# Kernel tuning notes

Measured on AMD Instinct MI355X. Metric: run time of the kernel, lower is better.

The kernel has to match this reference:

```python
import jax, jax.numpy as jnp
import numpy as np

DEGREE = 7

def setup_inputs() -> dict:
    key = jax.random.key(0)
    k1, k2 = jax.random.split(key)
    input_dims, output_dims = 1024, 1024
    x = jax.random.normal(k1, (8192, input_dims), dtype=jnp.float32)
    std = 1.0 / (input_dims * (DEGREE + 1))
    lucas_coeffs = std * jax.random.normal(k2, (input_dims, output_dims, DEGREE + 1), dtype=jnp.float32)
    return {"x": x, "lucas_coeffs": lucas_coeffs}

def reference(x, lucas_coeffs):
    input_dims = lucas_coeffs.shape[0]
    x = x.reshape(-1, input_dims)
    x = jnp.tanh(x)
    # Lucas polynomial recurrence: L0=2, L1=x, L_i = x*L_{i-1} + L_{i-2}
    basis = [jnp.full_like(x, 2.0)]
    if DEGREE > 0:
        basis.append(x)
    for i in range(2, DEGREE + 1):
        basis.append(x * basis[-1] + basis[-2])
    lucas = jnp.stack(basis, axis=-1)  # [b, i, d]
    y = jnp.einsum('bid,iod->bo', lucas, lucas_coeffs)
    return y
```

## Files before the change

### kernel.cpp

```cpp
#include <hip/hip_runtime.h>
#include <hip/hip_bf16.h>


typedef __attribute__((ext_vector_type(8)))  short  short8;
typedef __attribute__((ext_vector_type(4)))  unsigned short ushort4v;
typedef __attribute__((ext_vector_type(8)))  unsigned short ushort8;
typedef __attribute__((ext_vector_type(4)))  float  float4v;
typedef __attribute__((ext_vector_type(4)))  unsigned int uint4v;

#define M_DIM 8192
#define I_DIM 1024
#define O_DIM 1024
#define K_DIM 8192
#define BM 64
#define BN 128
#define BK 64
#define NSTEP (K_DIM / BK)

__device__ __forceinline__ unsigned short f2bf(float f) {
    unsigned int u = __float_as_uint(f);
    u += 0x7FFFu + ((u >> 16) & 1u);
    return (unsigned short)(u >> 16);
}

__global__ __launch_bounds__(256) void prep_t_kernel(const float* __restrict__ x,
                                                     unsigned short* __restrict__ T) {
    int idx = (blockIdx.x * 256 + threadIdx.x) * 4;
    float4v v = *(const float4v*)(x + idx);
    ushort4v o;
    o[0] = f2bf(tanhf(v[0]));
    o[1] = f2bf(tanhf(v[1]));
    o[2] = f2bf(tanhf(v[2]));
    o[3] = f2bf(tanhf(v[3]));
    *(ushort4v*)(T + idx) = o;
}

__global__ __launch_bounds__(256) void prep_b_kernel(const float* __restrict__ c,
                                                     unsigned short* __restrict__ Bt) {
    int idx = blockIdx.x * 256 + threadIdx.x;
    int i = idx >> 10;
    int o = idx & 1023;
    const float* src = c + (size_t)i * 8192 + o * 8;
    float4v lo = *(const float4v*)(src);
    float4v hi = *(const float4v*)(src + 4);
    ushort8 v;
    v[0] = f2bf(lo[0]); v[1] = f2bf(lo[1]); v[2] = f2bf(lo[2]); v[3] = f2bf(lo[3]);
    v[4] = f2bf(hi[0]); v[5] = f2bf(hi[1]); v[6] = f2bf(hi[2]); v[7] = f2bf(hi[3]);
    *(ushort8*)(Bt + (size_t)o * K_DIM + i * 8) = v;
}

__device__ __forceinline__ short8 lucas_frag(unsigned int tb) {
    const float t = __uint_as_float(tb << 16);
    const float L2v = fmaf(t, t, 2.0f);
    const float L3v = fmaf(t, L2v, t);
    const float L4v = fmaf(t, L3v, L2v);
    const float L5v = fmaf(t, L4v, L3v);
    const float L6v = fmaf(t, L5v, L4v);
    const float L7v = fmaf(t, L6v, L5v);
    const unsigned int u2 = __float_as_uint(L2v) + 0x8000u;
    const unsigned int u3 = __float_as_uint(L3v) + 0x8000u;
    const unsigned int u4 = __float_as_uint(L4v) + 0x8000u;
    const unsigned int u5 = __float_as_uint(L5v) + 0x8000u;
    const unsigned int u6 = __float_as_uint(L6v) + 0x8000u;
    const unsigned int u7 = __float_as_uint(L7v) + 0x8000u;
    union { uint4v u; short8 s; } r;
    r.u[0] = 0x4000u | (tb << 16);
    r.u[1] = __builtin_amdgcn_perm(u3, u2, 0x07060302);
    r.u[2] = __builtin_amdgcn_perm(u5, u4, 0x07060302);
    r.u[3] = __builtin_amdgcn_perm(u7, u6, 0x07060302);
    return r.s;
}

__global__ __launch_bounds__(256, 4) void gemm_kernel(const unsigned short* __restrict__ T,
                                                      const unsigned short* __restrict__ Bt,
                                                      float* __restrict__ out) {
    __shared__ unsigned short Bs[2][BN * BK];
    __shared__ unsigned short Ts[2][BM * 8];

    const int tid  = threadIdx.x;
    const int lane = tid & 63;
    const int wave = tid >> 6;
    const int m0 = blockIdx.x * BM;
    const int n0 = blockIdx.y * BN;

    const int wm0  = (wave >> 1) * 32;
    const int wn0  = (wave & 1) * 64;
    const int l16  = lane & 15;
    const int quad = lane >> 4;

    const int srow   = lane >> 3;
    const int il     = lane & 7;
    const int gchunk = il ^ srow;

    float4v acc[2][4];
    const float4v zero = {0.f, 0.f, 0.f, 0.f};
    #pragma unroll
    for (int a = 0; a < 2; ++a)
        #pragma unroll
        for (int b = 0; b < 4; ++b) acc[a][b] = zero;

    #pragma unroll
    for (int r = 0; r < 4; ++r) {
        const int rowb = r * 32 + wave * 8;
        const unsigned short* gB = Bt + (size_t)(n0 + rowb + srow) * K_DIM + gchunk * 8;
        __builtin_amdgcn_global_load_lds(
            (const __attribute__((address_space(1))) unsigned int*)gB,
            (__attribute__((address_space(3))) unsigned int*)&Bs[0][rowb * BK], 16, 0, 0);
    }
    if (wave == 0) {
        const unsigned short* gT = T + (size_t)(m0 + lane) * I_DIM;
        __builtin_amdgcn_global_load_lds(
            (const __attribute__((address_space(1))) unsigned int*)gT,
            (__attribute__((address_space(3))) unsigned int*)&Ts[0][0], 16, 0, 0);
    }
    __syncthreads();

    int cur = 0;
    for (int s = 0; s < NSTEP; ++s) {
        const int nxt = cur ^ 1;

        if (s + 1 < NSTEP) {
            const int kt = (s + 1) * BK;
            #pragma unroll
            for (int r = 0; r < 4; ++r) {
                const int rowb = r * 32 + wave * 8;
                const unsigned short* gB = Bt + (size_t)(n0 + rowb + srow) * K_DIM + kt + gchunk * 8;
                __builtin_amdgcn_global_load_lds(
                    (const __attribute__((address_space(1))) unsigned int*)gB,
                    (__attribute__((address_space(3))) unsigned int*)&Bs[nxt][rowb * BK], 16, 0, 0);
            }
            if (wave == 0) {
                const unsigned short* gT = T + (size_t)(m0 + lane) * I_DIM + kt / 8;
                __builtin_amdgcn_global_load_lds(
                    (const __attribute__((address_space(1))) unsigned int*)gT,
                    (__attribute__((address_space(3))) unsigned int*)&Ts[nxt][0], 16, 0, 0);
            }
        }

        unsigned int tb[2][2];
        #pragma unroll
        for (int tt = 0; tt < 2; ++tt)
            #pragma unroll
            for (int k2 = 0; k2 < 2; ++k2)
                tb[tt][k2] = Ts[cur][(wm0 + tt * 16 + l16) * 8 + (k2 * 4 + quad)];

        #pragma unroll
        for (int k2 = 0; k2 < 2; ++k2) {
            short8 af[2];
            af[0] = lucas_frag(tb[0][k2]);
            af[1] = lucas_frag(tb[1][k2]);
            short8 bfr[4];
            #pragma unroll
            for (int tn = 0; tn < 4; ++tn) {
                const int brow = wn0 + tn * 16 + l16;
                bfr[tn] = *(const short8*)&Bs[cur][brow * BK + (((k2 * 4 + quad) ^ (l16 & 7)) * 8)];
            }
            #pragma unroll
            for (int tt = 0; tt < 2; ++tt)
                #pragma unroll
                for (int tn = 0; tn < 4; ++tn)
                    acc[tt][tn] = __builtin_amdgcn_mfma_f32_16x16x32_bf16(
                        af[tt], bfr[tn], acc[tt][tn], 0, 0, 0);
        }

        __syncthreads();
        cur = nxt;
    }

    #pragma unroll
    for (int tt = 0; tt < 2; ++tt) {
        #pragma unroll
        for (int tn = 0; tn < 4; ++tn) {
            const int col = n0 + wn0 + tn * 16 + l16;
            #pragma unroll
            for (int r = 0; r < 4; ++r) {
                const int row = m0 + wm0 + tt * 16 + quad * 4 + r;
                out[(size_t)row * O_DIM + col] = acc[tt][tn][r];
            }
        }
    }
}

__global__ __launch_bounds__(256) void naive_kernel(const float* __restrict__ x,
                                                    const float* __restrict__ c,
                                                    float* __restrict__ out) {
    int idx = blockIdx.x * 256 + threadIdx.x;
    int b = idx >> 10;
    int o = idx & 1023;
    const float* xb = x + (size_t)b * I_DIM;
    float acc = 0.f;
    for (int i = 0; i < I_DIM; ++i) {
        float t = tanhf(xb[i]);
        float L[8];
        L[0] = 2.0f; L[1] = t;
        #pragma unroll
        for (int d = 2; d < 8; ++d) L[d] = t * L[d - 1] + L[d - 2];
        const float* cc = c + (size_t)i * 8192 + o * 8;
        #pragma unroll
        for (int d = 0; d < 8; ++d) acc += L[d] * cc[d];
    }
    out[idx] = acc;
}

extern "C" void kernel_launch(void* const* d_in, const int* in_sizes, int n_in,
                              void* d_out, int out_size, void* d_ws, size_t ws_size,
                              hipStream_t stream) {
    const float* x      = (const float*)d_in[0];
    const float* coeffs = (const float*)d_in[1];
    float* out = (float*)d_out;

    const size_t btBytes = (size_t)O_DIM * K_DIM * sizeof(unsigned short);
    const size_t tBytes  = (size_t)M_DIM * I_DIM * sizeof(unsigned short);

    if (ws_size >= btBytes + tBytes) {
        unsigned short* Bt = (unsigned short*)d_ws;
        unsigned short* T  = (unsigned short*)((char*)d_ws + btBytes);

        prep_b_kernel<<<(I_DIM * O_DIM) / 256, 256, 0, stream>>>(coeffs, Bt);
        prep_t_kernel<<<(M_DIM * I_DIM) / (4 * 256), 256, 0, stream>>>(x, T);

        dim3 grid(M_DIM / BM, O_DIM / BN);
        gemm_kernel<<<grid, 256, 0, stream>>>(T, Bt, out);
    } else {
        naive_kernel<<<(M_DIM * O_DIM) / 256, 256, 0, stream>>>(x, coeffs, out);
    }
}
```

Baseline: 268.5 us.

## Fuse prep kernels, pack T pairs, use hardware bf16 convert, swap grid order

Merges the two preprocessing kernels into one launch, with the T part writing 8 values per thread interleaved so each lane reads both of its k-chunks with one 32-bit LDS load. Lucas fragment packing uses the hardware packed bf16 conversion when the builtin exists, replacing the add-and-permute truncation. The GEMM grid is transposed so consecutive blocks share the same T rows across N tiles, which changes L2 reuse. The goal is fewer launches, fewer LDS reads and ALU ops in the inner loop, at the cost of a more intricate T layout and a rounding mode that differs slightly from the old one.

```diff
diff --git a/kernel.cpp b/kernel.cpp
--- a/kernel.cpp
+++ b/kernel.cpp
@@ -23,30 +23,37 @@
     return (unsigned short)(u >> 16);
 }
 
-__global__ __launch_bounds__(256) void prep_t_kernel(const float* __restrict__ x,
-                                                     unsigned short* __restrict__ T) {
-    int idx = (blockIdx.x * 256 + threadIdx.x) * 4;
-    float4v v = *(const float4v*)(x + idx);
-    ushort4v o;
-    o[0] = f2bf(tanhf(v[0]));
-    o[1] = f2bf(tanhf(v[1]));
-    o[2] = f2bf(tanhf(v[2]));
-    o[3] = f2bf(tanhf(v[3]));
-    *(ushort4v*)(T + idx) = o;
-}
-
-__global__ __launch_bounds__(256) void prep_b_kernel(const float* __restrict__ c,
-                                                     unsigned short* __restrict__ Bt) {
-    int idx = blockIdx.x * 256 + threadIdx.x;
-    int i = idx >> 10;
-    int o = idx & 1023;
-    const float* src = c + (size_t)i * 8192 + o * 8;
-    float4v lo = *(const float4v*)(src);
-    float4v hi = *(const float4v*)(src + 4);
-    ushort8 v;
-    v[0] = f2bf(lo[0]); v[1] = f2bf(lo[1]); v[2] = f2bf(lo[2]); v[3] = f2bf(lo[3]);
-    v[4] = f2bf(hi[0]); v[5] = f2bf(hi[1]); v[6] = f2bf(hi[2]); v[7] = f2bf(hi[3]);
-    *(ushort8*)(Bt + (size_t)o * K_DIM + i * 8) = v;
+__global__ __launch_bounds__(256) void prep_kernel(const float* __restrict__ x,
+                                                   const float* __restrict__ c,
+                                                   unsigned short* __restrict__ T,
+                                                   unsigned short* __restrict__ Bt) {
+    int bid = blockIdx.x;
+    const int tPart = (M_DIM * I_DIM) / (8 * 256);
+    if (bid < tPart) {
+        int idx = (bid * 256 + threadIdx.x) * 8;
+        float4v v0 = *(const float4v*)(x + idx);
+        float4v v1 = *(const float4v*)(x + idx + 4);
+        unsigned short t[8];
+        t[0] = f2bf(tanhf(v0[0])); t[1] = f2bf(tanhf(v0[1]));
+        t[2] = f2bf(tanhf(v0[2])); t[3] = f2bf(tanhf(v0[3]));
+        t[4] = f2bf(tanhf(v1[0])); t[5] = f2bf(tanhf(v1[1]));
+        t[6] = f2bf(tanhf(v1[2])); t[7] = f2bf(tanhf(v1[3]));
+        ushort8 o;
+        #pragma unroll
+        for (int p = 0; p < 4; ++p) { o[2 * p] = t[p]; o[2 * p + 1] = t[p + 4]; }
+        *(ushort8*)(T + idx) = o;
+    } else {
+        int idx = (bid - tPart) * 256 + threadIdx.x;
+        int i = idx >> 10;
+        int o = idx & 1023;
+        const float* src = c + (size_t)i * 8192 + o * 8;
+        float4v lo = *(const float4v*)(src);
+        float4v hi = *(const float4v*)(src + 4);
+        ushort8 v;
+        v[0] = f2bf(lo[0]); v[1] = f2bf(lo[1]); v[2] = f2bf(lo[2]); v[3] = f2bf(lo[3]);
+        v[4] = f2bf(hi[0]); v[5] = f2bf(hi[1]); v[6] = f2bf(hi[2]); v[7] = f2bf(hi[3]);
+        *(ushort8*)(Bt + (size_t)o * K_DIM + i * 8) = v;
+    }
 }
 
 __device__ __forceinline__ short8 lucas_frag(unsigned int tb) {
@@ -57,17 +64,26 @@
     const float L5v = fmaf(t, L4v, L3v);
     const float L6v = fmaf(t, L5v, L4v);
     const float L7v = fmaf(t, L6v, L5v);
-    const unsigned int u2 = __float_as_uint(L2v) + 0x8000u;
-    const unsigned int u3 = __float_as_uint(L3v) + 0x8000u;
-    const unsigned int u4 = __float_as_uint(L4v) + 0x8000u;
-    const unsigned int u5 = __float_as_uint(L5v) + 0x8000u;
-    const unsigned int u6 = __float_as_uint(L6v) + 0x8000u;
-    const unsigned int u7 = __float_as_uint(L7v) + 0x8000u;
     union { uint4v u; short8 s; } r;
-    r.u[0] = 0x4000u | (tb << 16);
-    r.u[1] = __builtin_amdgcn_perm(u3, u2, 0x07060302);
-    r.u[2] = __builtin_amdgcn_perm(u5, u4, 0x07060302);
-    r.u[3] = __builtin_amdgcn_perm(u7, u6, 0x07060302);
+#if __has_builtin(__builtin_amdgcn_cvt_pk_bf16_f32)
+    {
+        auto p0 = __builtin_amdgcn_cvt_pk_bf16_f32(2.0f, t);
+        auto p1 = __builtin_amdgcn_cvt_pk_bf16_f32(L2v, L3v);
+        auto p2 = __builtin_amdgcn_cvt_pk_bf16_f32(L4v, L5v);
+        auto p3 = __builtin_amdgcn_cvt_pk_bf16_f32(L6v, L7v);
+        __builtin_memcpy(&r.u[0], &p0, 4);
+        __builtin_memcpy(&r.u[1], &p1, 4);
+        __builtin_memcpy(&r.u[2], &p2, 4);
+        __builtin_memcpy(&r.u[3], &p3, 4);
+    }
+#else
+    {
+        r.u[0] = 0x4000u | (tb << 16);
+        r.u[1] = __builtin_amdgcn_perm(__float_as_uint(L3v), __float_as_uint(L2v), 0x07060302);
+        r.u[2] = __builtin_amdgcn_perm(__float_as_uint(L5v), __float_as_uint(L4v), 0x07060302);
+        r.u[3] = __builtin_amdgcn_perm(__float_as_uint(L7v), __float_as_uint(L6v), 0x07060302);
+    }
+#endif
     return r.s;
 }
 
@@ -80,8 +96,8 @@
     const int tid  = threadIdx.x;
     const int lane = tid & 63;
     const int wave = tid >> 6;
-    const int m0 = blockIdx.x * BM;
-    const int n0 = blockIdx.y * BN;
+    const int n0 = blockIdx.x * BN;
+    const int m0 = blockIdx.y * BM;
 
     const int wm0  = (wave >> 1) * 32;
     const int wn0  = (wave & 1) * 64;
@@ -137,18 +153,16 @@
             }
         }
 
-        unsigned int tb[2][2];
+        unsigned int tw[2];
         #pragma unroll
         for (int tt = 0; tt < 2; ++tt)
-            #pragma unroll
-            for (int k2 = 0; k2 < 2; ++k2)
-                tb[tt][k2] = Ts[cur][(wm0 + tt * 16 + l16) * 8 + (k2 * 4 + quad)];
+            tw[tt] = *(const unsigned int*)&Ts[cur][(wm0 + tt * 16 + l16) * 8 + quad * 2];
 
         #pragma unroll
         for (int k2 = 0; k2 < 2; ++k2) {
             short8 af[2];
-            af[0] = lucas_frag(tb[0][k2]);
-            af[1] = lucas_frag(tb[1][k2]);
+            af[0] = lucas_frag(k2 ? (tw[0] >> 16) : (tw[0] & 0xffffu));
+            af[1] = lucas_frag(k2 ? (tw[1] >> 16) : (tw[1] & 0xffffu));
             short8 bfr[4];
             #pragma unroll
             for (int tn = 0; tn < 4; ++tn) {
@@ -216,10 +230,11 @@
         unsigned short* Bt = (unsigned short*)d_ws;
         unsigned short* T  = (unsigned short*)((char*)d_ws + btBytes);
 
-        prep_b_kernel<<<(I_DIM * O_DIM) / 256, 256, 0, stream>>>(coeffs, Bt);
-        prep_t_kernel<<<(M_DIM * I_DIM) / (4 * 256), 256, 0, stream>>>(x, T);
-
-        dim3 grid(M_DIM / BM, O_DIM / BN);
+        const int tBlocks = (M_DIM * I_DIM) / (8 * 256);
+        const int bBlocks = (I_DIM * O_DIM) / 256;
+        prep_kernel<<<tBlocks + bBlocks, 256, 0, stream>>>(x, coeffs, T, Bt);
+
+        dim3 grid(O_DIM / BN, M_DIM / BM);
         gemm_kernel<<<grid, 256, 0, stream>>>(T, Bt, out);
     } else {
         naive_kernel<<<(M_DIM * O_DIM) / 256, 256, 0, stream>>>(x, coeffs, out);
```

Result: faster. 254.3 us (-5.3%).
